# Performance work log

Hardware: AMD Instinct MI355X
Metric: run time of the kernel (lower is better)

## Reference

```python
import jax, jax.numpy as jnp
import numpy as np

NUM_HEADS = 16
HEAD_DIM = 128
ROPE_BASE = 10000.0


def rotate_half(x):
    x1, x2 = jnp.split(x, 2, axis=-1)
    return jnp.concatenate((-x2, x1), axis=-1)


def rope_cos_sin(seq_len, dim, dtype):
    inv_freq = 1.0 / (ROPE_BASE ** (jnp.arange(0, dim, 2, dtype=jnp.float32) / dim))
    t = jnp.arange(seq_len, dtype=jnp.float32)
    freqs = jnp.einsum('i,j->ij', t, inv_freq)          # [S, dim/2]
    emb = jnp.concatenate((freqs, freqs), axis=-1)       # [S, dim]
    return emb.astype(dtype)  # caller applies cos/sin


def setup_inputs() -> dict:
    key = jax.random.key(0)
    k0, k1, k2, k3, k4 = jax.random.split(key, 5)
    B, S, H = 2, 2048, 2048
    hd = H // NUM_HEADS
    scale = 0.02
    return {
        'hidden_states': jax.random.normal(k0, (B, S, H), dtype=jnp.float32),
        'Wq': jax.random.normal(k1, (H, H), dtype=jnp.float32) * scale,
        'Wk': jax.random.normal(k2, (hd, H), dtype=jnp.float32) * scale,
        'Wv': jax.random.normal(k3, (hd, H), dtype=jnp.float32) * scale,
        'Wo': jax.random.normal(k4, (H, H), dtype=jnp.float32) * scale,
    }


def reference(hidden_states, Wq, Wk, Wv, Wo):
    B, S, H = hidden_states.shape
    nH, hd = NUM_HEADS, HEAD_DIM

    # projections (torch Linear: x @ W.T)
    q = jnp.einsum('bsh,oh->bso', hidden_states, Wq).reshape(B, S, nH, hd)
    q = q.transpose(0, 2, 1, 3)                          # [B, nH, S, hd]
    k = jnp.einsum('bsh,dh->bsd', hidden_states, Wk)      # [B, S, hd] single KV head
    v = jnp.einsum('bsh,dh->bsd', hidden_states, Wv)      # [B, S, hd]

    # rotary embedding
    emb = rope_cos_sin(S, hd, hidden_states.dtype)        # [S, hd]
    cos, sin = jnp.cos(emb), jnp.sin(emb)
    q = q * cos[None, None] + rotate_half(q) * sin[None, None]
    k = k * cos[None] + rotate_half(k) * sin[None]

    # attention: Q heads against shared K/V head
    scores = jnp.einsum('bhqd,bkd->bhqk', q, k) / jnp.sqrt(jnp.asarray(hd, hidden_states.dtype))
    attn = jax.nn.softmax(scores, axis=-1)               # dropout is identity in eval
    out = jnp.einsum('bhqk,bkd->bhqd', attn, v)           # [B, nH, S, hd]
    out = out.transpose(0, 2, 1, 3).reshape(B, S, H)
    attn_output = jnp.einsum('bsh,oh->bso', out, Wo)

    # cache tensors returned by the torch module: k, v with head dim of 1
    return attn_output, k[:, None], v[:, None]
```

## Files before the change

### kernel.cpp

```cpp
#include <hip/hip_runtime.h>
#include <hip/hip_bf16.h>

typedef __hip_bfloat16 bf16;

#define NH   16
#define HD   128
#define SEQ  2048
#define BB   2
#define HID  2048

#define ROPE_C 0.14391156856f

using frag  = __attribute__((ext_vector_type(8))) short;
using f32x4 = __attribute__((ext_vector_type(4))) float;


__device__ __forceinline__ void cvt8_store(const float4 f0, const float4 f1, bf16* dst) {
    union { frag v; bf16 h[8]; } p;
    p.h[0] = __float2bfloat16(f0.x); p.h[1] = __float2bfloat16(f0.y);
    p.h[2] = __float2bfloat16(f0.z); p.h[3] = __float2bfloat16(f0.w);
    p.h[4] = __float2bfloat16(f1.x); p.h[5] = __float2bfloat16(f1.y);
    p.h[6] = __float2bfloat16(f1.z); p.h[7] = __float2bfloat16(f1.w);
    *reinterpret_cast<frag*>(dst) = p.v;
}

__device__ __forceinline__ unsigned pk2(float a, float b) {
    union { bf16 h[2]; unsigned u; } p;
    p.h[0] = __float2bfloat16(a);
    p.h[1] = __float2bfloat16(b);
    return p.u;
}

__global__ __launch_bounds__(512) void gemm_qkv(const float* __restrict__ A,
                                                const float* __restrict__ Wq,
                                                const float* __restrict__ Wk,
                                                const float* __restrict__ Wv,
                                                bf16* __restrict__ qout,
                                                float* __restrict__ Ck,
                                                float* __restrict__ Cv,
                                                bf16* __restrict__ kb,
                                                bf16* __restrict__ vt) {
    __shared__ bf16 Asl[4096];
    __shared__ bf16 Bsl[4096];
    const int tid  = threadIdx.x;
    const int wave = tid >> 6;
    const int lane = tid & 63;
    const int quad = lane >> 4;
    const int l15  = lane & 15;
    const int row0 = blockIdx.y * 128;
    const int bx   = blockIdx.x;
    const bool isq  = bx < 16;
    const bool is_v = (bx == 17);
    const float* W  = isq ? Wq : (is_v ? Wv : Wk);
    const int col0  = isq ? bx * 128 : 0;

    const int sr = tid >> 2;
    const int sc = (tid & 3) * 8;

    f32x4 acc[8];
#pragma unroll
    for (int j = 0; j < 8; ++j) acc[j] = (f32x4){0.f,0.f,0.f,0.f};

    for (int k0 = 0; k0 < HID; k0 += 32) {
        __syncthreads();
        {
            const float4* a0 = reinterpret_cast<const float4*>(A + (size_t)(row0 + sr) * HID + k0 + sc);
            const float4* b0 = reinterpret_cast<const float4*>(W + (size_t)(col0 + sr) * HID + k0 + sc);
            cvt8_store(a0[0], a0[1], &Asl[tid * 8]);
            cvt8_store(b0[0], b0[1], &Bsl[tid * 8]);
        }
        __syncthreads();
        frag af, bfr[8];
        af = *reinterpret_cast<const frag*>(&Asl[(((wave*16 + l15)*4) + quad) * 8]);
#pragma unroll
        for (int j = 0; j < 8; ++j)
            bfr[j] = *reinterpret_cast<const frag*>(&Bsl[(((j*16 + l15)*4) + quad) * 8]);
#pragma unroll
        for (int j = 0; j < 8; ++j)
            acc[j] = __builtin_amdgcn_mfma_f32_16x16x32_bf16(af, bfr[j], acc[j], 0, 0, 0);
    }

    if (isq) {
#pragma unroll
        for (int r = 0; r < 4; ++r) {
            const int row = row0 + wave*16 + quad*4 + r;
            const int s = row & (SEQ - 1);
            bf16* crow = qout + (size_t)row * HID + col0;
#pragma unroll
            for (int j = 0; j < 4; ++j) {
                const int d = 16*j + l15;
                const float invf = expf(-(float)d * ROPE_C);
                float sn, cs;
                sincosf((float)s * invf, &sn, &cs);
                const float x1 = acc[j][r], x2 = acc[j+4][r];
                crow[d]      = __float2bfloat16(x1*cs - x2*sn);
                crow[d + 64] = __float2bfloat16(x2*cs + x1*sn);
            }
        }
    } else if (is_v) {
#pragma unroll
        for (int r = 0; r < 4; ++r) {
            const int row = row0 + wave*16 + quad*4 + r;
            const int s = row & (SEQ - 1);
            const int b = row >> 11;
            float* crow = Cv + (size_t)row * HD;
#pragma unroll
            for (int j = 0; j < 8; ++j) {
                const int d = 16*j + l15;
                const float val = acc[j][r];
                crow[d] = val;
                vt[((size_t)b * HD + d) * SEQ + s] = __float2bfloat16(val);
            }
        }
    } else {
#pragma unroll
        for (int r = 0; r < 4; ++r) {
            const int row = row0 + wave*16 + quad*4 + r;
            const int s = row & (SEQ - 1);
            float* crow = Ck + (size_t)row * HD;
#pragma unroll
            for (int j = 0; j < 4; ++j) {
                const int d = 16*j + l15;
                const float invf = expf(-(float)d * ROPE_C);
                float sn, cs;
                sincosf((float)s * invf, &sn, &cs);
                const float y1 = acc[j][r]*cs - acc[j+4][r]*sn;
                const float y2 = acc[j+4][r]*cs + acc[j][r]*sn;
                crow[d]      = y1;
                crow[d + 64] = y2;
                kb[(size_t)row * HD + d]      = __float2bfloat16(y1);
                kb[(size_t)row * HD + d + 64] = __float2bfloat16(y2);
            }
        }
    }
}

__global__ __launch_bounds__(256) void attn_mfma(const bf16* __restrict__ qbuf,
                                                 const bf16* __restrict__ kb,
                                                 const bf16* __restrict__ vt,
                                                 bf16* __restrict__ attn_out) {
    __shared__ bf16 Ks[8192];
    __shared__ bf16 Vt[8192];

    const int tid  = threadIdx.x;
    const int wave = tid >> 6;
    const int lane = tid & 63;
    const int quad = lane >> 4;
    const int l15  = lane & 15;
    const int q0   = blockIdx.x * 64;
    const int h    = blockIdx.y;
    const int b    = blockIdx.z;

    const bf16* kbb = kb + (size_t)b * SEQ * HD;
    const bf16* vtb = vt + (size_t)b * HD * SEQ;

    frag qfr[4];
    {
        const bf16* qrow = qbuf + ((size_t)(b * SEQ + q0 + wave * 16 + l15)) * HID + h * HD;
#pragma unroll
        for (int c = 0; c < 4; ++c)
            qfr[c] = *reinterpret_cast<const frag*>(qrow + c * 32 + quad * 8);
    }

    int kkey[4], kdim[4], kof[4];
#pragma unroll
    for (int i = 0; i < 4; ++i) {
        const int n = tid + i * 256;
        kkey[i] = ((n >> 2) & 15) + (((n >> 6) & 3) << 4);
        kdim[i] = ((n >> 8) << 5) + ((n & 3) << 3);
        kof[i]  = (n * 16) ^ (((n >> 3) & 7) << 4);
    }
    int vdim[8], vkey[8], vof[8];
#pragma unroll
    for (int i = 0; i < 8; ++i) {
        const int m = tid + i * 256;
        vdim[i] = ((m >> 8) << 4) + ((m >> 3) & 15);
        vkey[i] = (((m >> 7) & 1) << 5) + ((m & 1) << 4) + (((m >> 1) & 3) << 2);
        vof[i]  = (m * 8) ^ (((m >> 4) & 7) << 4);
    }

    const int rb  = (l15 * 4 + quad) * 16;
    const int rbs = rb ^ (((rb >> 7) & 7) << 4);

    f32x4 oacc[8];
#pragma unroll
    for (int dt = 0; dt < 8; ++dt) oacc[dt] = (f32x4){0.f, 0.f, 0.f, 0.f};
    float mrow = -1e30f;
    float lrow = 0.f;
    const float scale = 0.088388347648318433f;

    for (int t0 = 0; t0 < SEQ; t0 += 64) {
        __syncthreads();
        {
            uint4 krg[4];
            uint2 vrg[8];
#pragma unroll
            for (int i = 0; i < 4; ++i)
                krg[i] = *reinterpret_cast<const uint4*>(kbb + (size_t)(t0 + kkey[i]) * HD + kdim[i]);
#pragma unroll
            for (int i = 0; i < 8; ++i)
                vrg[i] = *reinterpret_cast<const uint2*>(vtb + (size_t)vdim[i] * SEQ + t0 + vkey[i]);
#pragma unroll
            for (int i = 0; i < 4; ++i)
                *reinterpret_cast<uint4*>(reinterpret_cast<char*>(Ks) + kof[i]) = krg[i];
#pragma unroll
            for (int i = 0; i < 8; ++i)
                *reinterpret_cast<uint2*>(reinterpret_cast<char*>(Vt) + vof[i]) = vrg[i];
        }
        __syncthreads();

        f32x4 sacc[4];
#pragma unroll
        for (int t = 0; t < 4; ++t) sacc[t] = (f32x4){0.f,0.f,0.f,0.f};
#pragma unroll
        for (int c = 0; c < 4; ++c) {
            frag kf[4];
#pragma unroll
            for (int t = 0; t < 4; ++t)
                kf[t] = *reinterpret_cast<const frag*>(
                            reinterpret_cast<const char*>(Ks) + (c*4+t)*1024 + rbs);
#pragma unroll
            for (int t = 0; t < 4; ++t)
                sacc[t] = __builtin_amdgcn_mfma_f32_16x16x32_bf16(kf[t], qfr[c], sacc[t], 0, 0, 0);
        }

        float mx = -1e30f;
#pragma unroll
        for (int t = 0; t < 4; ++t)
#pragma unroll
            for (int r = 0; r < 4; ++r) mx = fmaxf(mx, sacc[t][r]);
        mx = fmaxf(mx, __shfl_xor(mx, 16));
        mx = fmaxf(mx, __shfl_xor(mx, 32));
        const bool skip = (bool)__all(mx - mrow <= 90.0f);
        const float mn = skip ? mrow : fmaxf(mrow, mx);
        const float al = skip ? 1.f : __expf((mrow - mn) * scale);
        float p[4][4];
        float ps = 0.f;
#pragma unroll
        for (int t = 0; t < 4; ++t)
#pragma unroll
            for (int r = 0; r < 4; ++r) {
                p[t][r] = __expf((sacc[t][r] - mn) * scale);
                ps += p[t][r];
            }
        ps += __shfl_xor(ps, 16);
        ps += __shfl_xor(ps, 32);
        lrow = lrow * al + ps;
        mrow = mn;

        frag pb[2];
#pragma unroll
        for (int hh = 0; hh < 2; ++hh) {
            union { unsigned u[4]; frag f; } pf;
            pf.u[0] = pk2(p[2*hh][0],   p[2*hh][1]);
            pf.u[1] = pk2(p[2*hh][2],   p[2*hh][3]);
            pf.u[2] = pk2(p[2*hh+1][0], p[2*hh+1][1]);
            pf.u[3] = pk2(p[2*hh+1][2], p[2*hh+1][3]);
            pb[hh] = pf.f;
        }

        if (!skip)
#pragma unroll
            for (int dt = 0; dt < 8; ++dt)
#pragma unroll
                for (int r = 0; r < 4; ++r) oacc[dt][r] *= al;

#pragma unroll
        for (int dt = 0; dt < 8; ++dt) {
            frag v0 = *reinterpret_cast<const frag*>(
                          reinterpret_cast<const char*>(Vt) + (dt*2+0)*1024 + rbs);
            frag v1 = *reinterpret_cast<const frag*>(
                          reinterpret_cast<const char*>(Vt) + (dt*2+1)*1024 + rbs);
            oacc[dt] = __builtin_amdgcn_mfma_f32_16x16x32_bf16(v0, pb[0], oacc[dt], 0, 0, 0);
            oacc[dt] = __builtin_amdgcn_mfma_f32_16x16x32_bf16(v1, pb[1], oacc[dt], 0, 0, 0);
        }
    }

    {
        const float inv = 1.f / lrow;
        const int s = q0 + wave * 16 + l15;
        bf16* orow = attn_out + ((size_t)(b * SEQ + s)) * HID + h * HD;
#pragma unroll
        for (int dt = 0; dt < 8; ++dt) {
            uint2 val;
            val.x = pk2(oacc[dt][0] * inv, oacc[dt][1] * inv);
            val.y = pk2(oacc[dt][2] * inv, oacc[dt][3] * inv);
            *reinterpret_cast<uint2*>(orow + dt * 16 + quad * 4) = val;
        }
    }
}

__global__ __launch_bounds__(512) void gemm_o_mfma(const bf16* __restrict__ A,
                                                   const float* __restrict__ W,
                                                   float* __restrict__ C) {
    __shared__ bf16 Asl[4096];
    __shared__ bf16 Bsl[4096];
    const int tid  = threadIdx.x;
    const int wave = tid >> 6;
    const int lane = tid & 63;
    const int quad = lane >> 4;
    const int l15  = lane & 15;
    const int row0 = blockIdx.y * 128;
    const int col0 = blockIdx.x * 128;

    const int sr = tid >> 2;
    const int sc = (tid & 3) * 8;

    f32x4 acc[8];
#pragma unroll
    for (int j = 0; j < 8; ++j) acc[j] = (f32x4){0.f,0.f,0.f,0.f};

    for (int k0 = 0; k0 < HID; k0 += 32) {
        __syncthreads();
        {
            *reinterpret_cast<uint4*>(&Asl[tid * 8]) =
                *reinterpret_cast<const uint4*>(A + (size_t)(row0 + sr) * HID + k0 + sc);
            const float4* b0 = reinterpret_cast<const float4*>(W + (size_t)(col0 + sr) * HID + k0 + sc);
            cvt8_store(b0[0], b0[1], &Bsl[tid * 8]);
        }
        __syncthreads();
        frag af, bfr[8];
        af = *reinterpret_cast<const frag*>(&Asl[(((wave*16 + l15)*4) + quad) * 8]);
#pragma unroll
        for (int j = 0; j < 8; ++j)
            bfr[j] = *reinterpret_cast<const frag*>(&Bsl[(((j*16 + l15)*4) + quad) * 8]);
#pragma unroll
        for (int j = 0; j < 8; ++j)
            acc[j] = __builtin_amdgcn_mfma_f32_16x16x32_bf16(af, bfr[j], acc[j], 0, 0, 0);
    }

#pragma unroll
    for (int r = 0; r < 4; ++r) {
        const int row = row0 + wave*16 + quad*4 + r;
        float* crow = C + (size_t)row * HID + col0;
#pragma unroll
        for (int j = 0; j < 8; ++j)
            crow[16*j + l15] = acc[j][r];
    }
}

extern "C" void kernel_launch(void* const* d_in, const int* in_sizes, int n_in,
                              void* d_out, int out_size, void* d_ws, size_t ws_size,
                              hipStream_t stream) {
    const float* hs = (const float*)d_in[0];
    const float* Wq = (const float*)d_in[1];
    const float* Wk = (const float*)d_in[2];
    const float* Wv = (const float*)d_in[3];
    const float* Wo = (const float*)d_in[4];

    float* out      = (float*)d_out;
    float* out_attn = out;
    float* out_k    = out + 8388608;
    float* out_v    = out + 8388608 + 524288;

    bf16* qbuf = (bf16*)d_out;
    bf16* kb   = (bf16*)((char*)d_out + 16777216);
    bf16* vt   = (bf16*)((char*)d_out + 17825792);
    bf16* attn_out = (bf16*)d_ws;

    gemm_qkv  <<<dim3(18, (BB*SEQ)/128), dim3(512), 0, stream>>>(hs, Wq, Wk, Wv,
                                                                 qbuf, out_k, out_v, kb, vt);
    attn_mfma <<<dim3(SEQ/64, NH, BB),   dim3(256), 0, stream>>>(qbuf, kb, vt, attn_out);
    gemm_o_mfma<<<dim3(HID/128, (BB*SEQ)/128), dim3(512), 0, stream>>>(attn_out, Wo, out_attn);
}
```

Baseline: 405.9 us.

## Switch attention kernel to 32x32x16 MFMA tiles with two-wave blocks

Rewrites the attention kernel to use 32x32x16 bf16 MFMA instructions, with each wave covering 32 query rows instead of 16, and halves the block to 128 threads. The K/V shared-memory staging layout is rebuilt to match the new fragment layout. The larger tiles mean fewer MFMA issues and fewer LDS fragment reads per FLOP, and the row max/sum reductions need one fewer cross-lane shuffle. In exchange there is higher register pressure (larger accumulators, 8 Q fragments), and the new unswizzled LDS layout may cause bank conflicts.

```diff
diff --git a/kernel.cpp b/kernel.cpp
--- a/kernel.cpp
+++ b/kernel.cpp
@@ -11,8 +11,9 @@
 
 #define ROPE_C 0.14391156856f
 
-using frag  = __attribute__((ext_vector_type(8))) short;
-using f32x4 = __attribute__((ext_vector_type(4))) float;
+using frag   = __attribute__((ext_vector_type(8))) short;
+using f32x4  = __attribute__((ext_vector_type(4))) float;
+using f32x16 = __attribute__((ext_vector_type(16))) float;
 
 
 __device__ __forceinline__ void cvt8_store(const float4 f0, const float4 f1, bf16* dst) {
@@ -135,7 +136,7 @@
     }
 }
 
-__global__ __launch_bounds__(256) void attn_mfma(const bf16* __restrict__ qbuf,
+__global__ __launch_bounds__(128) void attn_mfma(const bf16* __restrict__ qbuf,
                                                  const bf16* __restrict__ kb,
                                                  const bf16* __restrict__ vt,
                                                  bf16* __restrict__ attn_out) {
@@ -145,46 +146,43 @@
     const int tid  = threadIdx.x;
     const int wave = tid >> 6;
     const int lane = tid & 63;
-    const int quad = lane >> 4;
-    const int l15  = lane & 15;
+    const int l31  = lane & 31;
+    const int h    = lane >> 5;
     const int q0   = blockIdx.x * 64;
-    const int h    = blockIdx.y;
+    const int hh   = blockIdx.y;
     const int b    = blockIdx.z;
 
     const bf16* kbb = kb + (size_t)b * SEQ * HD;
     const bf16* vtb = vt + (size_t)b * HD * SEQ;
 
-    frag qfr[4];
+    frag qfr[8];
     {
-        const bf16* qrow = qbuf + ((size_t)(b * SEQ + q0 + wave * 16 + l15)) * HID + h * HD;
-#pragma unroll
-        for (int c = 0; c < 4; ++c)
-            qfr[c] = *reinterpret_cast<const frag*>(qrow + c * 32 + quad * 8);
-    }
-
-    int kkey[4], kdim[4], kof[4];
-#pragma unroll
-    for (int i = 0; i < 4; ++i) {
-        const int n = tid + i * 256;
-        kkey[i] = ((n >> 2) & 15) + (((n >> 6) & 3) << 4);
-        kdim[i] = ((n >> 8) << 5) + ((n & 3) << 3);
-        kof[i]  = (n * 16) ^ (((n >> 3) & 7) << 4);
-    }
-    int vdim[8], vkey[8], vof[8];
+        const bf16* qrow = qbuf + ((size_t)(b * SEQ + q0 + wave * 32 + l31)) * HID + hh * HD;
+#pragma unroll
+        for (int c = 0; c < 8; ++c)
+            qfr[c] = *reinterpret_cast<const frag*>(qrow + c * 16 + h * 8);
+    }
+
+    int koff[8], voff[8];
 #pragma unroll
     for (int i = 0; i < 8; ++i) {
-        const int m = tid + i * 256;
-        vdim[i] = ((m >> 8) << 4) + ((m >> 3) & 15);
-        vkey[i] = (((m >> 7) & 1) << 5) + ((m & 1) << 4) + (((m >> 1) & 3) << 2);
-        vof[i]  = (m * 8) ^ (((m >> 4) & 7) << 4);
-    }
-
-    const int rb  = (l15 * 4 + quad) * 16;
-    const int rbs = rb ^ (((rb >> 7) & 7) << 4);
-
-    f32x4 oacc[8];
-#pragma unroll
-    for (int dt = 0; dt < 8; ++dt) oacc[dt] = (f32x4){0.f, 0.f, 0.f, 0.f};
+        const int n  = tid + i * 128;
+        const int kl = (n >> 1) & 31, khs = n & 1;
+        const int key  = ((n >> 9) << 5) + kl;
+        const int dimb = (((n >> 6) & 7) << 4) + (khs << 3);
+        koff[i] = key * HD + dimb;
+        const int ks  = (n >> 6) & 3;
+        const int dim = ((n >> 8) << 5) + kl;
+        const int kA  = ((ks >> 1) << 5) + ((ks & 1) << 4) + (khs << 2);
+        voff[i] = dim * SEQ + kA;
+    }
+    const int rpos = (l31 * 2 + h) * 16;
+
+    f32x16 oacc[4];
+#pragma unroll
+    for (int dt = 0; dt < 4; ++dt)
+#pragma unroll
+        for (int r = 0; r < 16; ++r) oacc[dt][r] = 0.f;
     float mrow = -1e30f;
     float lrow = 0.f;
     const float scale = 0.088388347648318433f;
@@ -192,101 +190,107 @@
     for (int t0 = 0; t0 < SEQ; t0 += 64) {
         __syncthreads();
         {
-            uint4 krg[4];
-            uint2 vrg[8];
-#pragma unroll
-            for (int i = 0; i < 4; ++i)
-                krg[i] = *reinterpret_cast<const uint4*>(kbb + (size_t)(t0 + kkey[i]) * HD + kdim[i]);
+            uint4 krg[8];
+            const bf16* kt0 = kbb + (size_t)t0 * HD;
 #pragma unroll
             for (int i = 0; i < 8; ++i)
-                vrg[i] = *reinterpret_cast<const uint2*>(vtb + (size_t)vdim[i] * SEQ + t0 + vkey[i]);
-#pragma unroll
-            for (int i = 0; i < 4; ++i)
-                *reinterpret_cast<uint4*>(reinterpret_cast<char*>(Ks) + kof[i]) = krg[i];
+                krg[i] = *reinterpret_cast<const uint4*>(kt0 + koff[i]);
 #pragma unroll
             for (int i = 0; i < 8; ++i)
-                *reinterpret_cast<uint2*>(reinterpret_cast<char*>(Vt) + vof[i]) = vrg[i];
-        }
-        __syncthreads();
-
-        f32x4 sacc[4];
-#pragma unroll
-        for (int t = 0; t < 4; ++t) sacc[t] = (f32x4){0.f,0.f,0.f,0.f};
-#pragma unroll
-        for (int c = 0; c < 4; ++c) {
-            frag kf[4];
-#pragma unroll
-            for (int t = 0; t < 4; ++t)
-                kf[t] = *reinterpret_cast<const frag*>(
-                            reinterpret_cast<const char*>(Ks) + (c*4+t)*1024 + rbs);
-#pragma unroll
-            for (int t = 0; t < 4; ++t)
-                sacc[t] = __builtin_amdgcn_mfma_f32_16x16x32_bf16(kf[t], qfr[c], sacc[t], 0, 0, 0);
+                *reinterpret_cast<uint4*>(reinterpret_cast<char*>(Ks) + (tid + i*128) * 16) = krg[i];
+            uint4 vrg[8];
+            const bf16* vt0 = vtb + t0;
+#pragma unroll
+            for (int i = 0; i < 8; ++i) {
+                const uint2 a = *reinterpret_cast<const uint2*>(vt0 + voff[i]);
+                const uint2 c = *reinterpret_cast<const uint2*>(vt0 + voff[i] + 8);
+                vrg[i] = (uint4){a.x, a.y, c.x, c.y};
+            }
+#pragma unroll
+            for (int i = 0; i < 8; ++i)
+                *reinterpret_cast<uint4*>(reinterpret_cast<char*>(Vt) + (tid + i*128) * 16) = vrg[i];
+        }
+        __syncthreads();
+
+        f32x16 sacc[2];
+#pragma unroll
+        for (int kt = 0; kt < 2; ++kt)
+#pragma unroll
+            for (int r = 0; r < 16; ++r) sacc[kt][r] = 0.f;
+#pragma unroll
+        for (int c = 0; c < 8; ++c) {
+            const frag kf0 = *reinterpret_cast<const frag*>(
+                reinterpret_cast<const char*>(Ks) + (0*8 + c) * 1024 + rpos);
+            const frag kf1 = *reinterpret_cast<const frag*>(
+                reinterpret_cast<const char*>(Ks) + (1*8 + c) * 1024 + rpos);
+            sacc[0] = __builtin_amdgcn_mfma_f32_32x32x16_bf16(kf0, qfr[c], sacc[0], 0, 0, 0);
+            sacc[1] = __builtin_amdgcn_mfma_f32_32x32x16_bf16(kf1, qfr[c], sacc[1], 0, 0, 0);
         }
 
         float mx = -1e30f;
 #pragma unroll
-        for (int t = 0; t < 4; ++t)
-#pragma unroll
-            for (int r = 0; r < 4; ++r) mx = fmaxf(mx, sacc[t][r]);
-        mx = fmaxf(mx, __shfl_xor(mx, 16));
+        for (int kt = 0; kt < 2; ++kt)
+#pragma unroll
+            for (int r = 0; r < 16; ++r) mx = fmaxf(mx, sacc[kt][r]);
         mx = fmaxf(mx, __shfl_xor(mx, 32));
         const bool skip = (bool)__all(mx - mrow <= 90.0f);
         const float mn = skip ? mrow : fmaxf(mrow, mx);
         const float al = skip ? 1.f : __expf((mrow - mn) * scale);
-        float p[4][4];
+        float p[2][16];
         float ps = 0.f;
 #pragma unroll
-        for (int t = 0; t < 4; ++t)
-#pragma unroll
-            for (int r = 0; r < 4; ++r) {
-                p[t][r] = __expf((sacc[t][r] - mn) * scale);
-                ps += p[t][r];
-            }
-        ps += __shfl_xor(ps, 16);
+        for (int kt = 0; kt < 2; ++kt)
+#pragma unroll
+            for (int r = 0; r < 16; ++r) {
+                p[kt][r] = __expf((sacc[kt][r] - mn) * scale);
+                ps += p[kt][r];
+            }
         ps += __shfl_xor(ps, 32);
         lrow = lrow * al + ps;
         mrow = mn;
 
-        frag pb[2];
-#pragma unroll
-        for (int hh = 0; hh < 2; ++hh) {
+        frag pb[4];
+#pragma unroll
+        for (int ks = 0; ks < 4; ++ks) {
+            const int kt = ks >> 1, ta = (ks & 1) * 2, tb = ta + 1;
             union { unsigned u[4]; frag f; } pf;
-            pf.u[0] = pk2(p[2*hh][0],   p[2*hh][1]);
-            pf.u[1] = pk2(p[2*hh][2],   p[2*hh][3]);
-            pf.u[2] = pk2(p[2*hh+1][0], p[2*hh+1][1]);
-            pf.u[3] = pk2(p[2*hh+1][2], p[2*hh+1][3]);
-            pb[hh] = pf.f;
+            pf.u[0] = pk2(p[kt][ta*4+0], p[kt][ta*4+1]);
+            pf.u[1] = pk2(p[kt][ta*4+2], p[kt][ta*4+3]);
+            pf.u[2] = pk2(p[kt][tb*4+0], p[kt][tb*4+1]);
+            pf.u[3] = pk2(p[kt][tb*4+2], p[kt][tb*4+3]);
+            pb[ks] = pf.f;
         }
 
         if (!skip)
 #pragma unroll
-            for (int dt = 0; dt < 8; ++dt)
-#pragma unroll
-                for (int r = 0; r < 4; ++r) oacc[dt][r] *= al;
-
-#pragma unroll
-        for (int dt = 0; dt < 8; ++dt) {
-            frag v0 = *reinterpret_cast<const frag*>(
-                          reinterpret_cast<const char*>(Vt) + (dt*2+0)*1024 + rbs);
-            frag v1 = *reinterpret_cast<const frag*>(
-                          reinterpret_cast<const char*>(Vt) + (dt*2+1)*1024 + rbs);
-            oacc[dt] = __builtin_amdgcn_mfma_f32_16x16x32_bf16(v0, pb[0], oacc[dt], 0, 0, 0);
-            oacc[dt] = __builtin_amdgcn_mfma_f32_16x16x32_bf16(v1, pb[1], oacc[dt], 0, 0, 0);
+            for (int dt = 0; dt < 4; ++dt)
+#pragma unroll
+                for (int r = 0; r < 16; ++r) oacc[dt][r] *= al;
+
+#pragma unroll
+        for (int dt = 0; dt < 4; ++dt) {
+#pragma unroll
+            for (int ks = 0; ks < 4; ++ks) {
+                const frag vf = *reinterpret_cast<const frag*>(
+                    reinterpret_cast<const char*>(Vt) + (dt*4 + ks) * 1024 + rpos);
+                oacc[dt] = __builtin_amdgcn_mfma_f32_32x32x16_bf16(vf, pb[ks], oacc[dt], 0, 0, 0);
+            }
         }
     }
 
     {
         const float inv = 1.f / lrow;
-        const int s = q0 + wave * 16 + l15;
-        bf16* orow = attn_out + ((size_t)(b * SEQ + s)) * HID + h * HD;
-#pragma unroll
-        for (int dt = 0; dt < 8; ++dt) {
-            uint2 val;
-            val.x = pk2(oacc[dt][0] * inv, oacc[dt][1] * inv);
-            val.y = pk2(oacc[dt][2] * inv, oacc[dt][3] * inv);
-            *reinterpret_cast<uint2*>(orow + dt * 16 + quad * 4) = val;
-        }
+        const int s = q0 + wave * 32 + l31;
+        bf16* orow = attn_out + ((size_t)(b * SEQ + s)) * HID + hh * HD;
+#pragma unroll
+        for (int dt = 0; dt < 4; ++dt)
+#pragma unroll
+            for (int t = 0; t < 4; ++t) {
+                uint2 val;
+                val.x = pk2(oacc[dt][t*4+0] * inv, oacc[dt][t*4+1] * inv);
+                val.y = pk2(oacc[dt][t*4+2] * inv, oacc[dt][t*4+3] * inv);
+                *reinterpret_cast<uint2*>(orow + dt*32 + t*8 + h*4) = val;
+            }
     }
 }
 
@@ -360,6 +364,6 @@
 
     gemm_qkv  <<<dim3(18, (BB*SEQ)/128), dim3(512), 0, stream>>>(hs, Wq, Wk, Wv,
                                                                  qbuf, out_k, out_v, kb, vt);
-    attn_mfma <<<dim3(SEQ/64, NH, BB),   dim3(256), 0, stream>>>(qbuf, kb, vt, attn_out);
+    attn_mfma <<<dim3(SEQ/64, NH, BB),   dim3(128), 0, stream>>>(qbuf, kb, vt, attn_out);
     gemm_o_mfma<<<dim3(HID/128, (BB*SEQ)/128), dim3(512), 0, stream>>>(attn_out, Wo, out_attn);
 }
```

New measurement: 433.9 us. 1.07x slower.
